# Optimization experiments

Hardware: AMD Instinct MI355X
Metric: run time of the kernel (lower is better)

## Reference

```python
import jax, jax.numpy as jnp
import numpy as np

NUM_HEADS = 32
MAX_BIAS_LENGTH = 1024
ROPE_BASE = 10000.0


def _rope_cos_sin(seq_len, head_dim, dtype):
    half = head_dim // 2
    inv_freq = 1.0 / (ROPE_BASE ** (jnp.arange(0, half, dtype=jnp.float32) / half))
    t = jnp.arange(seq_len, dtype=jnp.float32)
    freqs = jnp.outer(t, inv_freq)  # [S, half]
    return jnp.cos(freqs).astype(dtype), jnp.sin(freqs).astype(dtype)


def _apply_rope(x, cos, sin):
    # x: [B, S, H, D]; non-interleaved (GPT-NeoX / flash-attn style) rotary
    half = x.shape[-1] // 2
    x1, x2 = x[..., :half], x[..., half:]
    c = cos[None, :, None, :]
    s = sin[None, :, None, :]
    return jnp.concatenate([x1 * c - x2 * s, x1 * s + x2 * c], axis=-1)


def setup_inputs() -> dict:
    key = jax.random.key(0)
    ks = jax.random.split(key, 7)
    B, S, Dm = 2, 2048, 2048
    std = 1.0 / np.sqrt(Dm)
    return {
        "hidden_states": jax.random.normal(ks[0], (B, S, Dm), jnp.float32),
        "Wq": jax.random.normal(ks[1], (Dm, Dm), jnp.float32) * std,
        "Wk": jax.random.normal(ks[2], (Dm, Dm), jnp.float32) * std,
        "Wv": jax.random.normal(ks[3], (Dm, Dm), jnp.float32) * std,
        "Wo": jax.random.normal(ks[4], (Dm, Dm), jnp.float32) * std,
        "learnable_bias": jax.random.normal(ks[5], (NUM_HEADS, MAX_BIAS_LENGTH), jnp.float32) * 0.001,
        "softmax_offset": jnp.zeros((NUM_HEADS,), jnp.float32),
    }


def reference(hidden_states, Wq, Wk, Wv, Wo, learnable_bias, softmax_offset):
    B, S, Dm = hidden_states.shape
    H = NUM_HEADS
    D = Dm // H
    scale = D ** -0.5

    # projections (nn.Linear: x @ W.T)
    q = (hidden_states @ Wq.T).reshape(B, S, H, D)
    k = (hidden_states @ Wk.T).reshape(B, S, H, D)
    v = (hidden_states @ Wv.T).reshape(B, S, H, D)

    cos, sin = _rope_cos_sin(S, D, q.dtype)
    q = _apply_rope(q, cos, sin)
    k = _apply_rope(k, cos, sin)

    q = q.transpose(0, 2, 1, 3)  # [B, H, S, D]
    k = k.transpose(0, 2, 1, 3)
    v = v.transpose(0, 2, 1, 3)

    scores = jnp.einsum("bhid,bhjd->bhij", q, k) * scale  # [B, H, S, S]

    # per-diagonal learnable bias: diag = i - j in [0, MAX_BIAS_LENGTH)
    i = jnp.arange(S)[:, None]
    j = jnp.arange(S)[None, :]
    diag = i - j  # [S, S]
    causal = diag >= 0
    in_band = causal & (diag < MAX_BIAS_LENGTH)
    bias = jnp.where(in_band, learnable_bias[:, jnp.clip(diag, 0, MAX_BIAS_LENGTH - 1)], 0.0)  # [H, S, S]
    scores = scores + bias[None]
    scores = jnp.where(causal[None, None], scores, -jnp.inf)

    # softmax with learnable per-head offset (attention-sink logit)
    off = softmax_offset[None, :, None]  # [1, H, 1]
    m = jnp.maximum(jnp.max(scores, axis=-1), off)  # [B, H, S]
    p = jnp.exp(scores - m[..., None])
    denom = jnp.sum(p, axis=-1) + jnp.exp(off - m)  # [B, H, S]
    out = jnp.einsum("bhij,bhjd->bhid", p, v) / denom[..., None]

    out = out.transpose(0, 2, 1, 3).reshape(B, S, Dm)
    return out @ Wo.T
```

## Files before the change

### kernel.cpp

```cpp
#include <hip/hip_runtime.h>
#include <hip/hip_bf16.h>
#include <stdint.h>

typedef __bf16 bf16x8 __attribute__((ext_vector_type(8)));
typedef float f32x4 __attribute__((ext_vector_type(4)));
typedef unsigned short u16;
typedef u16 u16x4 __attribute__((ext_vector_type(4)));

#define S_LEN 2048
#define DMODEL 2048
#define NHEADS 32
#define BATCH 2
#define MROWS (BATCH * S_LEN)
#define BIAS_LEN 1024
#define LOG2E 1.44269504088896f

__device__ __forceinline__ u16 b16(float f) {
  union { __bf16 h; u16 u; } cv; cv.h = (__bf16)f; return cv.u;
}

__device__ __forceinline__ void gload16(const void* g, void* l) {
  __builtin_amdgcn_global_load_lds(
      (const __attribute__((address_space(1))) uint32_t*)g,
      (__attribute__((address_space(3))) uint32_t*)l, 16, 0, 0);
}

__global__ __launch_bounds__(256)
void prep_all(const float* __restrict__ hs,
              const float* __restrict__ w0, const float* __restrict__ w1,
              const float* __restrict__ w2, const float* __restrict__ w3,
              const float* __restrict__ bias,
              u16* __restrict__ hs_b, u16* __restrict__ w_b,
              float* __restrict__ ct, float* __restrict__ st,
              u16* __restrict__ b16t)
{
  const int blk = blockIdx.x;
  if (blk < 8192) {
    int i = (blk * 256 + threadIdx.x) * 4;
    float4 v = *(const float4*)(hs + i);
    u16x4 o = { b16(v.x), b16(v.y), b16(v.z), b16(v.w) };
    *(u16x4*)(hs_b + i) = o;
  } else if (blk < 24576) {
    int r = blk - 8192;
    int which = r >> 12;
    const float* src = (which == 0) ? w0 : (which == 1) ? w1
                     : (which == 2) ? w2 : w3;
    int i = ((r & 4095) * 256 + threadIdx.x) * 4;
    float4 v = *(const float4*)(src + i);
    u16x4 o = { b16(v.x), b16(v.y), b16(v.z), b16(v.w) };
    *(u16x4*)(w_b + (size_t)which * DMODEL * DMODEL + i) = o;
  } else if (blk < 24832) {
    int idx = (blk - 24576) * 256 + threadIdx.x;
    int s = idx >> 5, d = idx & 31;
    float inv = exp2f((float)d * (-13.287712379549449f / 32.0f));
    float a = (float)s * inv;
    ct[idx] = cosf(a);
    st[idx] = sinf(a);
  } else {
    int i = (blk - 24832) * 256 + threadIdx.x;
    b16t[i] = b16(bias[i] * LOG2E);
  }
}

#define GEMM_MAIN_LOOP(Aptr, Bptr)                                            \
  f32x4 acc[4][4] = {};                                                       \
  const u16* aS[4]; const u16* bS[4];                                         \
  _Pragma("unroll")                                                           \
  for (int it = 0; it < 4; ++it) {                                            \
    int u = it * 256 + tid;                                                   \
    int row = u >> 3;                                                         \
    int ch  = (u & 7) ^ (row & 7);                                            \
    aS[it] = (Aptr) + (size_t)(tm + row) * DMODEL + ch * 8;                   \
    bS[it] = (Bptr) + (size_t)(tn + row) * DMODEL + ch * 8;                   \
  }                                                                           \
  for (int k0 = 0; k0 < DMODEL; k0 += 64) {                                   \
    __syncthreads();                                                          \
    _Pragma("unroll")                                                         \
    for (int it = 0; it < 4; ++it) {                                          \
      int u = it * 256 + tid;                                                 \
      gload16(aS[it] + k0, (char*)sA + u * 16);                               \
      gload16(bS[it] + k0, (char*)sB + u * 16);                               \
    }                                                                         \
    __syncthreads();                                                          \
    _Pragma("unroll")                                                         \
    for (int kk = 0; kk < 2; ++kk) {                                          \
      bf16x8 af[4], bq[4];                                                    \
      _Pragma("unroll")                                                       \
      for (int mi = 0; mi < 4; ++mi) {                                        \
        int row = wm * 64 + mi * 16 + lc;                                     \
        int ch  = (kk * 4 + lr) ^ (row & 7);                                  \
        af[mi] = *(const bf16x8*)((const char*)sA + row * 128 + ch * 16);     \
      }                                                                       \
      _Pragma("unroll")                                                       \
      for (int ni = 0; ni < 4; ++ni) {                                        \
        int row = wn * 64 + ni * 16 + lc;                                     \
        int ch  = (kk * 4 + lr) ^ (row & 7);                                  \
        bq[ni] = *(const bf16x8*)((const char*)sB + row * 128 + ch * 16);     \
      }                                                                       \
      _Pragma("unroll")                                                       \
      for (int mi = 0; mi < 4; ++mi)                                          \
        _Pragma("unroll")                                                     \
        for (int ni = 0; ni < 4; ++ni)                                        \
          acc[mi][ni] = __builtin_amdgcn_mfma_f32_16x16x32_bf16(              \
              af[mi], bq[ni], acc[mi][ni], 0, 0, 0);                          \
    }                                                                         \
  }

__global__ __launch_bounds__(256)
void gemm_qkv(const u16* __restrict__ A, const u16* __restrict__ W,
              u16* __restrict__ qf, u16* __restrict__ kf, u16* __restrict__ vt,
              const float* __restrict__ ctab, const float* __restrict__ stab)
{
  __shared__ u16 sA[128 * 64];
  __shared__ u16 sB[128 * 64];
  const int tid  = threadIdx.x;
  const int lane = tid & 63;
  const int wid  = tid >> 6;
  const int wm   = wid >> 1, wn = wid & 1;
  const int lc   = lane & 15, lr = lane >> 4;
  const int L = blockIdx.x;
  const int r = L >> 3;
  const int x = (L & 7) * 6 + (r % 6);
  const int y = r / 6;
  const int which = x >> 4;
  const int tn = (x & 15) * 128;
  const int tm = y * 128;
  const u16* Bm = W + (size_t)which * DMODEL * DMODEL;

  GEMM_MAIN_LOOP(A, Bm)

  if (which == 2) {
    u16* C = vt;
#pragma unroll
    for (int mi = 0; mi < 4; ++mi)
#pragma unroll
      for (int ni = 0; ni < 4; ++ni) {
        int col = tn + wn * 64 + ni * 16 + lc;
        int hh = col >> 6, d = col & 63;
        int m0 = tm + wm * 64 + mi * 16 + lr * 4;
        int bb = m0 >> 11, s = m0 & 2047;
        u16x4 v = { b16(acc[mi][ni][0]), b16(acc[mi][ni][1]),
                    b16(acc[mi][ni][2]), b16(acc[mi][ni][3]) };
        *(u16x4*)(C + (((size_t)bb * NHEADS + hh) * 64 + d) * S_LEN + s) = v;
      }
  } else {
    u16* C = (which == 0) ? qf : kf;
    const float scl = (which == 0) ? 0.125f * LOG2E : 1.0f;
#pragma unroll
    for (int mi = 0; mi < 4; ++mi)
#pragma unroll
      for (int ni = 0; ni < 2; ++ni)
#pragma unroll
        for (int j = 0; j < 4; ++j) {
          int col = tn + wn * 64 + ni * 16 + lc;
          int hh = col >> 6, dl = col & 63;
          int rr2 = tm + wm * 64 + mi * 16 + lr * 4 + j;
          int bb = rr2 >> 11, s = rr2 & 2047;
          float x1 = acc[mi][ni][j], x2 = acc[mi][ni + 2][j];
          float cv = ctab[s * 32 + dl], sv = stab[s * 32 + dl];
          float o1 = (x1 * cv - x2 * sv) * scl;
          float o2 = (x1 * sv + x2 * cv) * scl;
          size_t base = (((size_t)bb * NHEADS + hh) * S_LEN + s) * 64 + dl;
          C[base]      = b16(o1);
          C[base + 32] = b16(o2);
        }
  }
}

__global__ __launch_bounds__(256)
void gemm_out(const u16* __restrict__ A, const u16* __restrict__ Bm,
              float* __restrict__ C)
{
  __shared__ u16 sA[128 * 64];
  __shared__ u16 sB[128 * 64];
  const int tid  = threadIdx.x;
  const int lane = tid & 63;
  const int wid  = tid >> 6;
  const int wm   = wid >> 1, wn = wid & 1;
  const int lc   = lane & 15, lr = lane >> 4;
  const int L = blockIdx.x;
  const int r = L >> 3;
  const int x = (L & 7) * 2 + (r & 1);
  const int y = r >> 1;
  const int tn = x * 128;
  const int tm = y * 128;

  GEMM_MAIN_LOOP(A, Bm)

#pragma unroll
  for (int mi = 0; mi < 4; ++mi)
#pragma unroll
    for (int ni = 0; ni < 4; ++ni)
#pragma unroll
      for (int j = 0; j < 4; ++j) {
        int rr2 = tm + wm * 64 + mi * 16 + lr * 4 + j;
        int c = tn + wn * 64 + ni * 16 + lc;
        C[(size_t)rr2 * DMODEL + c] = acc[mi][ni][j];
      }
}

__global__ __launch_bounds__(512, 6)
void attn_kernel(const u16* __restrict__ Q, const u16* __restrict__ K,
                 const u16* __restrict__ V, const u16* __restrict__ bias16,
                 const float* __restrict__ offg, u16* __restrict__ O)
{
  __shared__ __align__(16) u16 sK[2][64 * 64];
  __shared__ __align__(16) u16 sV[2][64 * 64];
  __shared__ __align__(16) u16 sP[8][16 * 72];
  __shared__ __align__(8)  u16 sBiasT[1152];

  const int tid = threadIdx.x, lane = tid & 63, wid = tid >> 6;
  const int lc = lane & 15, lr = lane >> 4;
  const int L  = blockIdx.x;
  const int p  = 15 - (L >> 6);
  const int bh = L & 63;
  const int h  = bh & 31;
  const int b  = bh >> 5;
  const int qw = p * 128 + wid * 16;
  const int nt = 2 * p + 2;

  for (int i = tid; i < 1152; i += 512) {
    int dd = i - 64;
    sBiasT[i] = (dd >= 0 && dd < BIAS_LEN) ? bias16[h * BIAS_LEN + dd] : (u16)0;
  }
  const float off = offg[h] * LOG2E;

  const u16* qp = Q + ((size_t)bh * S_LEN + qw + lc) * 64;
  bf16x8 aq0 = *(const bf16x8*)(qp + lr * 8);
  bf16x8 aq1 = *(const bf16x8*)(qp + 32 + lr * 8);

  const int srow = tid >> 3;
  const int sch  = (tid & 7) ^ (srow & 7);
  const u16* kSrc = K + ((size_t)bh * S_LEN + srow) * 64 + sch * 8;
  const u16* vSrc = V + ((size_t)bh * 64 + srow) * S_LEN + sch * 8;

  int offK[4][2], offV[2][4];
#pragma unroll
  for (int f = 0; f < 4; ++f) {
    int row = f * 16 + lc;
    offK[f][0] = row * 128 + ((lr) ^ (row & 7)) * 16;
    offK[f][1] = row * 128 + ((4 + lr) ^ (row & 7)) * 16;
  }
#pragma unroll
  for (int kk = 0; kk < 2; ++kk)
#pragma unroll
    for (int f2 = 0; f2 < 4; ++f2) {
      int drow = f2 * 16 + lc;
      offV[kk][f2] = drow * 128 + ((kk * 4 + lr) ^ (drow & 7)) * 16;
    }

  float lsum = 0.0f;
  f32x4 o[4] = {};

  gload16(kSrc, (char*)sK[0] + tid * 16);
  gload16(vSrc, (char*)sV[0] + tid * 16);
  __syncthreads();

  for (int t = 0; t < nt; ++t) {
    const int cur = t & 1;
    if (t + 1 < nt) {
      gload16(kSrc + (size_t)(t + 1) * 4096, (char*)sK[cur ^ 1] + tid * 16);
      gload16(vSrc + (t + 1) * 64,           (char*)sV[cur ^ 1] + tid * 16);
    }

    const int dqt = qw - t * 64;
    if (dqt >= 0) {
      const int db = dqt + lc;
      const bool inband = (dqt < 1088);
      f32x4 sc[4];
      __builtin_amdgcn_s_setprio(1);
#pragma unroll
      for (int f = 0; f < 4; ++f) {
        f32x4 z;
        if (inband) {
          const int ib = db + 64 - lr * 4 - f * 16;
#pragma unroll
          for (int j = 0; j < 4; ++j)
            z[j] = __uint_as_float((uint32_t)sBiasT[ib - j] << 16);
        } else {
          z[0] = z[1] = z[2] = z[3] = 0.0f;
        }
        bf16x8 k0 = *(const bf16x8*)((const char*)sK[cur] + offK[f][0]);
        bf16x8 k1 = *(const bf16x8*)((const char*)sK[cur] + offK[f][1]);
        z     = __builtin_amdgcn_mfma_f32_16x16x32_bf16(k0, aq0, z, 0, 0, 0);
        sc[f] = __builtin_amdgcn_mfma_f32_16x16x32_bf16(k1, aq1, z, 0, 0, 0);
      }
      __builtin_amdgcn_s_setprio(0);

      float pvv[4][4];
      if (dqt < 64) {
#pragma unroll
        for (int f = 0; f < 4; ++f)
#pragma unroll
          for (int j = 0; j < 4; ++j) {
            int dd = db - (f * 16 + lr * 4 + j);
            pvv[f][j] = (dd >= 0) ? sc[f][j] : -1e30f;
          }
      } else {
#pragma unroll
        for (int f = 0; f < 4; ++f)
#pragma unroll
          for (int j = 0; j < 4; ++j) pvv[f][j] = sc[f][j];
      }
#pragma unroll
      for (int f = 0; f < 4; ++f)
#pragma unroll
        for (int j = 0; j < 4; ++j) {
          float pe = exp2f(pvv[f][j]);
          pvv[f][j] = pe;
          lsum += pe;
        }

      u16* myP = sP[wid];
#pragma unroll
      for (int f = 0; f < 4; ++f) {
        u16x4 w = { b16(pvv[f][0]), b16(pvv[f][1]), b16(pvv[f][2]), b16(pvv[f][3]) };
        *(u16x4*)(myP + lc * 72 + f * 16 + lr * 4) = w;
      }
      asm volatile("s_waitcnt lgkmcnt(0)" ::: "memory");
      __builtin_amdgcn_sched_barrier(0);
      bf16x8 ap0 = *(const bf16x8*)(myP + lc * 72 + lr * 8);
      bf16x8 ap1 = *(const bf16x8*)(myP + lc * 72 + 32 + lr * 8);
      __builtin_amdgcn_s_setprio(1);
#pragma unroll
      for (int f2 = 0; f2 < 4; ++f2) {
        bf16x8 bv = *(const bf16x8*)((const char*)sV[cur] + offV[0][f2]);
        o[f2] = __builtin_amdgcn_mfma_f32_16x16x32_bf16(ap0, bv, o[f2], 0, 0, 0);
      }
#pragma unroll
      for (int f2 = 0; f2 < 4; ++f2) {
        bf16x8 bv = *(const bf16x8*)((const char*)sV[cur] + offV[1][f2]);
        o[f2] = __builtin_amdgcn_mfma_f32_16x16x32_bf16(ap1, bv, o[f2], 0, 0, 0);
      }
      __builtin_amdgcn_s_setprio(0);
    }
    __syncthreads();
  }

  lsum += __shfl_xor(lsum, 16, 64);
  lsum += __shfl_xor(lsum, 32, 64);
  lsum += exp2f(off);
  float ls[4];
#pragma unroll
  for (int j = 0; j < 4; ++j) ls[j] = 1.0f / __shfl(lsum, lr * 4 + j, 64);
#pragma unroll
  for (int f2 = 0; f2 < 4; ++f2)
#pragma unroll
    for (int j = 0; j < 4; ++j) {
      int i = qw + lr * 4 + j;
      int d = f2 * 16 + lc;
      size_t addr = (((size_t)(b * S_LEN + i)) * NHEADS + h) * 64 + d;
      O[addr] = b16(o[f2][j] * ls[j]);
    }
}

extern "C" void kernel_launch(void* const* d_in, const int* in_sizes, int n_in,
                              void* d_out, int out_size, void* d_ws, size_t ws_size,
                              hipStream_t stream)
{
  const float* hs   = (const float*)d_in[0];
  const float* Wq   = (const float*)d_in[1];
  const float* Wk   = (const float*)d_in[2];
  const float* Wv   = (const float*)d_in[3];
  const float* Wo   = (const float*)d_in[4];
  const float* bias = (const float*)d_in[5];
  const float* off  = (const float*)d_in[6];

  char* p = (char*)d_ws;
  u16* hs_b = (u16*)p; p += (size_t)MROWS * DMODEL * 2;
  u16* wq_b = (u16*)p; p += (size_t)DMODEL * DMODEL * 2;
  u16* wk_b = (u16*)p; p += (size_t)DMODEL * DMODEL * 2;
  u16* wv_b = (u16*)p; p += (size_t)DMODEL * DMODEL * 2;
  u16* wo_b = (u16*)p; p += (size_t)DMODEL * DMODEL * 2;
  u16* qf   = (u16*)p; p += (size_t)MROWS * DMODEL * 2;
  u16* kf   = (u16*)p; p += (size_t)MROWS * DMODEL * 2;
  u16* vt   = (u16*)p; p += (size_t)MROWS * DMODEL * 2;
  u16* att  = (u16*)p; p += (size_t)MROWS * DMODEL * 2;
  float* ct = (float*)p; p += (size_t)S_LEN * 32 * 4;
  float* st = (float*)p; p += (size_t)S_LEN * 32 * 4;
  u16* b16t = (u16*)p; p += (size_t)NHEADS * BIAS_LEN * 2;
  (void)ws_size; (void)in_sizes; (void)n_in; (void)out_size;
  (void)wk_b; (void)wv_b;

  prep_all<<<dim3(24960), 256, 0, stream>>>(hs, Wq, Wk, Wv, Wo, bias,
                                            hs_b, wq_b, ct, st, b16t);
  gemm_qkv<<<dim3(1536), 256, 0, stream>>>(hs_b, wq_b, qf, kf, vt, ct, st);
  attn_kernel<<<dim3(16 * 64), 512, 0, stream>>>(qf, kf, vt, b16t, off, att);
  gemm_out<<<dim3(512), 256, 0, stream>>>(att, wo_b, (float*)d_out);
}
```

Measured before the change: 274.3 us.

## Process two 128-row query groups per attention block to reuse K/V tiles

Each attention block now handles 256 query rows, split into two interleaved 128-row groups, so every wave computes two 16-row query tiles. Each K/V tile loaded into shared memory is reused by both groups, and the V fragments are read once and fed to both PV MFMAs. This halves the block count and cuts K/V global-to-LDS traffic per query. In exchange it raises register pressure (occupancy hint lowered from 6 to 4) and doubles the P scratch space. A scheduling remap pairs long and short causal rows.

```diff
diff --git a/kernel.cpp b/kernel.cpp
--- a/kernel.cpp
+++ b/kernel.cpp
@@ -199,25 +199,26 @@
       }
 }
 
-__global__ __launch_bounds__(512, 6)
+__global__ __launch_bounds__(512, 4)
 void attn_kernel(const u16* __restrict__ Q, const u16* __restrict__ K,
                  const u16* __restrict__ V, const u16* __restrict__ bias16,
                  const float* __restrict__ offg, u16* __restrict__ O)
 {
   __shared__ __align__(16) u16 sK[2][64 * 64];
   __shared__ __align__(16) u16 sV[2][64 * 64];
-  __shared__ __align__(16) u16 sP[8][16 * 72];
+  __shared__ __align__(16) u16 sP[16][16 * 72];
   __shared__ __align__(8)  u16 sBiasT[1152];
 
   const int tid = threadIdx.x, lane = tid & 63, wid = tid >> 6;
   const int lc = lane & 15, lr = lane >> 4;
   const int L  = blockIdx.x;
-  const int p  = 15 - (L >> 6);
+  const int sidx = L >> 6;
+  const int p  = (sidx < 4) ? 7 - sidx : sidx - 4;
   const int bh = L & 63;
   const int h  = bh & 31;
   const int b  = bh >> 5;
-  const int qw = p * 128 + wid * 16;
-  const int nt = 2 * p + 2;
+  const int qw0 = p * 256 + wid * 16;
+  const int nt = 4 * p + 4;
 
   for (int i = tid; i < 1152; i += 512) {
     int dd = i - 64;
@@ -225,9 +226,11 @@
   }
   const float off = offg[h] * LOG2E;
 
-  const u16* qp = Q + ((size_t)bh * S_LEN + qw + lc) * 64;
-  bf16x8 aq0 = *(const bf16x8*)(qp + lr * 8);
-  bf16x8 aq1 = *(const bf16x8*)(qp + 32 + lr * 8);
+  const u16* qp0 = Q + ((size_t)bh * S_LEN + qw0 + lc) * 64;
+  bf16x8 aq00 = *(const bf16x8*)(qp0 + lr * 8);
+  bf16x8 aq01 = *(const bf16x8*)(qp0 + 32 + lr * 8);
+  bf16x8 aq10 = *(const bf16x8*)(qp0 + 128 * 64 + lr * 8);
+  bf16x8 aq11 = *(const bf16x8*)(qp0 + 128 * 64 + 32 + lr * 8);
 
   const int srow = tid >> 3;
   const int sch  = (tid & 7) ^ (srow & 7);
@@ -249,12 +252,66 @@
       offV[kk][f2] = drow * 128 + ((kk * 4 + lr) ^ (drow & 7)) * 16;
     }
 
-  float lsum = 0.0f;
-  f32x4 o[4] = {};
+  float lsum0 = 0.0f, lsum1 = 0.0f;
+  f32x4 o0[4] = {}, o1[4] = {};
 
   gload16(kSrc, (char*)sK[0] + tid * 16);
   gload16(vSrc, (char*)sV[0] + tid * 16);
   __syncthreads();
+
+  auto do_group = [&](int dqt, const bf16x8& q0, const bf16x8& q1,
+                      u16* myP, float& lsum, const u16* sKc) {
+    const int db = dqt + lc;
+    const bool inband = (dqt < 1088);
+    f32x4 sc[4];
+    __builtin_amdgcn_s_setprio(1);
+#pragma unroll
+    for (int f = 0; f < 4; ++f) {
+      f32x4 z;
+      if (inband) {
+        const int ib = db + 64 - lr * 4 - f * 16;
+#pragma unroll
+        for (int j = 0; j < 4; ++j)
+          z[j] = __uint_as_float((uint32_t)sBiasT[ib - j] << 16);
+      } else {
+        z[0] = z[1] = z[2] = z[3] = 0.0f;
+      }
+      bf16x8 k0 = *(const bf16x8*)((const char*)sKc + offK[f][0]);
+      bf16x8 k1 = *(const bf16x8*)((const char*)sKc + offK[f][1]);
+      z     = __builtin_amdgcn_mfma_f32_16x16x32_bf16(k0, q0, z, 0, 0, 0);
+      sc[f] = __builtin_amdgcn_mfma_f32_16x16x32_bf16(k1, q1, z, 0, 0, 0);
+    }
+    __builtin_amdgcn_s_setprio(0);
+
+    float pvv[4][4];
+    if (dqt < 64) {
+#pragma unroll
+      for (int f = 0; f < 4; ++f)
+#pragma unroll
+        for (int j = 0; j < 4; ++j) {
+          int dd = db - (f * 16 + lr * 4 + j);
+          pvv[f][j] = (dd >= 0) ? sc[f][j] : -1e30f;
+        }
+    } else {
+#pragma unroll
+      for (int f = 0; f < 4; ++f)
+#pragma unroll
+        for (int j = 0; j < 4; ++j) pvv[f][j] = sc[f][j];
+    }
+#pragma unroll
+    for (int f = 0; f < 4; ++f)
+#pragma unroll
+      for (int j = 0; j < 4; ++j) {
+        float pe = exp2f(pvv[f][j]);
+        pvv[f][j] = pe;
+        lsum += pe;
+      }
+#pragma unroll
+    for (int f = 0; f < 4; ++f) {
+      u16x4 w = { b16(pvv[f][0]), b16(pvv[f][1]), b16(pvv[f][2]), b16(pvv[f][3]) };
+      *(u16x4*)(myP + lc * 72 + f * 16 + lr * 4) = w;
+    }
+  };
 
   for (int t = 0; t < nt; ++t) {
     const int cur = t & 1;
@@ -263,94 +320,63 @@
       gload16(vSrc + (t + 1) * 64,           (char*)sV[cur ^ 1] + tid * 16);
     }
 
-    const int dqt = qw - t * 64;
-    if (dqt >= 0) {
-      const int db = dqt + lc;
-      const bool inband = (dqt < 1088);
-      f32x4 sc[4];
+    const int dqt0 = qw0 - t * 64;
+    const int dqt1 = dqt0 + 128;
+    const bool a0 = (dqt0 >= 0), a1 = (dqt1 >= 0);
+
+    if (a1) do_group(dqt1, aq10, aq11, sP[wid * 2 + 1], lsum1, sK[cur]);
+    if (a0) do_group(dqt0, aq00, aq01, sP[wid * 2 + 0], lsum0, sK[cur]);
+
+    if (a1) {
+      asm volatile("s_waitcnt lgkmcnt(0)" ::: "memory");
+      __builtin_amdgcn_sched_barrier(0);
+      u16* P0 = sP[wid * 2 + 0];
+      u16* P1 = sP[wid * 2 + 1];
       __builtin_amdgcn_s_setprio(1);
 #pragma unroll
-      for (int f = 0; f < 4; ++f) {
-        f32x4 z;
-        if (inband) {
-          const int ib = db + 64 - lr * 4 - f * 16;
-#pragma unroll
-          for (int j = 0; j < 4; ++j)
-            z[j] = __uint_as_float((uint32_t)sBiasT[ib - j] << 16);
-        } else {
-          z[0] = z[1] = z[2] = z[3] = 0.0f;
+      for (int kk = 0; kk < 2; ++kk) {
+        bf16x8 bv[4];
+#pragma unroll
+        for (int f2 = 0; f2 < 4; ++f2)
+          bv[f2] = *(const bf16x8*)((const char*)sV[cur] + offV[kk][f2]);
+        bf16x8 ap1 = *(const bf16x8*)(P1 + lc * 72 + kk * 32 + lr * 8);
+#pragma unroll
+        for (int f2 = 0; f2 < 4; ++f2)
+          o1[f2] = __builtin_amdgcn_mfma_f32_16x16x32_bf16(ap1, bv[f2], o1[f2], 0, 0, 0);
+        if (a0) {
+          bf16x8 ap0 = *(const bf16x8*)(P0 + lc * 72 + kk * 32 + lr * 8);
+#pragma unroll
+          for (int f2 = 0; f2 < 4; ++f2)
+            o0[f2] = __builtin_amdgcn_mfma_f32_16x16x32_bf16(ap0, bv[f2], o0[f2], 0, 0, 0);
         }
-        bf16x8 k0 = *(const bf16x8*)((const char*)sK[cur] + offK[f][0]);
-        bf16x8 k1 = *(const bf16x8*)((const char*)sK[cur] + offK[f][1]);
-        z     = __builtin_amdgcn_mfma_f32_16x16x32_bf16(k0, aq0, z, 0, 0, 0);
-        sc[f] = __builtin_amdgcn_mfma_f32_16x16x32_bf16(k1, aq1, z, 0, 0, 0);
       }
       __builtin_amdgcn_s_setprio(0);
-
-      float pvv[4][4];
-      if (dqt < 64) {
-#pragma unroll
-        for (int f = 0; f < 4; ++f)
-#pragma unroll
-          for (int j = 0; j < 4; ++j) {
-            int dd = db - (f * 16 + lr * 4 + j);
-            pvv[f][j] = (dd >= 0) ? sc[f][j] : -1e30f;
-          }
-      } else {
-#pragma unroll
-        for (int f = 0; f < 4; ++f)
-#pragma unroll
-          for (int j = 0; j < 4; ++j) pvv[f][j] = sc[f][j];
-      }
-#pragma unroll
-      for (int f = 0; f < 4; ++f)
-#pragma unroll
-        for (int j = 0; j < 4; ++j) {
-          float pe = exp2f(pvv[f][j]);
-          pvv[f][j] = pe;
-          lsum += pe;
-        }
-
-      u16* myP = sP[wid];
-#pragma unroll
-      for (int f = 0; f < 4; ++f) {
-        u16x4 w = { b16(pvv[f][0]), b16(pvv[f][1]), b16(pvv[f][2]), b16(pvv[f][3]) };
-        *(u16x4*)(myP + lc * 72 + f * 16 + lr * 4) = w;
-      }
-      asm volatile("s_waitcnt lgkmcnt(0)" ::: "memory");
-      __builtin_amdgcn_sched_barrier(0);
-      bf16x8 ap0 = *(const bf16x8*)(myP + lc * 72 + lr * 8);
-      bf16x8 ap1 = *(const bf16x8*)(myP + lc * 72 + 32 + lr * 8);
-      __builtin_amdgcn_s_setprio(1);
-#pragma unroll
-      for (int f2 = 0; f2 < 4; ++f2) {
-        bf16x8 bv = *(const bf16x8*)((const char*)sV[cur] + offV[0][f2]);
-        o[f2] = __builtin_amdgcn_mfma_f32_16x16x32_bf16(ap0, bv, o[f2], 0, 0, 0);
-      }
-#pragma unroll
-      for (int f2 = 0; f2 < 4; ++f2) {
-        bf16x8 bv = *(const bf16x8*)((const char*)sV[cur] + offV[1][f2]);
-        o[f2] = __builtin_amdgcn_mfma_f32_16x16x32_bf16(ap1, bv, o[f2], 0, 0, 0);
-      }
-      __builtin_amdgcn_s_setprio(0);
     }
     __syncthreads();
   }
 
-  lsum += __shfl_xor(lsum, 16, 64);
-  lsum += __shfl_xor(lsum, 32, 64);
-  lsum += exp2f(off);
-  float ls[4];
-#pragma unroll
-  for (int j = 0; j < 4; ++j) ls[j] = 1.0f / __shfl(lsum, lr * 4 + j, 64);
+  lsum0 += __shfl_xor(lsum0, 16, 64);
+  lsum0 += __shfl_xor(lsum0, 32, 64);
+  lsum0 += exp2f(off);
+  lsum1 += __shfl_xor(lsum1, 16, 64);
+  lsum1 += __shfl_xor(lsum1, 32, 64);
+  lsum1 += exp2f(off);
+  float ls0[4], ls1[4];
+#pragma unroll
+  for (int j = 0; j < 4; ++j) {
+    ls0[j] = 1.0f / __shfl(lsum0, lr * 4 + j, 64);
+    ls1[j] = 1.0f / __shfl(lsum1, lr * 4 + j, 64);
+  }
 #pragma unroll
   for (int f2 = 0; f2 < 4; ++f2)
 #pragma unroll
     for (int j = 0; j < 4; ++j) {
-      int i = qw + lr * 4 + j;
+      int i0 = qw0 + lr * 4 + j;
       int d = f2 * 16 + lc;
-      size_t addr = (((size_t)(b * S_LEN + i)) * NHEADS + h) * 64 + d;
-      O[addr] = b16(o[f2][j] * ls[j]);
+      size_t a0d = (((size_t)(b * S_LEN + i0)) * NHEADS + h) * 64 + d;
+      O[a0d] = b16(o0[f2][j] * ls0[j]);
+      size_t a1d = (((size_t)(b * S_LEN + i0 + 128)) * NHEADS + h) * 64 + d;
+      O[a1d] = b16(o1[f2][j] * ls1[j]);
     }
 }
 
@@ -385,6 +411,6 @@
   prep_all<<<dim3(24960), 256, 0, stream>>>(hs, Wq, Wk, Wv, Wo, bias,
                                             hs_b, wq_b, ct, st, b16t);
   gemm_qkv<<<dim3(1536), 256, 0, stream>>>(hs_b, wq_b, qf, kf, vt, ct, st);
-  attn_kernel<<<dim3(16 * 64), 512, 0, stream>>>(qf, kf, vt, b16t, off, att);
+  attn_kernel<<<dim3(512), 512, 0, stream>>>(qf, kf, vt, b16t, off, att);
   gemm_out<<<dim3(512), 256, 0, stream>>>(att, wo_b, (float*)d_out);
 }
```

Result: no change. 276.3 us (+0.7%).

## Split QKV GEMM into 256x256 double-buffered Q/K kernel and separate V GEMM

Applied to the files above, without the earlier changes.

Replaces the single fused QKV projection kernel with a new Q/K GEMM that uses 256x256 tiles, 512 threads, a double-buffered LDS pipeline with explicit vmcnt/lgkmcnt waits, barriers and MFMA priority boosting. V is moved to its own 128x128 GEMM kernel. The aim is more data reuse per tile and better overlap of global loads with MFMA work. The cost is an extra kernel launch, large LDS use that limits occupancy, and only 256 blocks for the Q/K part, which may leave CUs underused.

```diff
diff --git a/kernel.cpp b/kernel.cpp
--- a/kernel.cpp
+++ b/kernel.cpp
@@ -60,6 +60,121 @@
     int i = (blk - 24832) * 256 + threadIdx.x;
     b16t[i] = b16(bias[i] * LOG2E);
   }
+}
+
+#define NT 32
+
+#define STG_A(buf, h, t) { \
+    gload16(aS0 + (size_t)(h) * 128 * DMODEL + (t) * 64, (char*)sA[buf][h] + tid * 16); \
+    gload16(aS0 + (size_t)((h) * 128 + 64) * DMODEL + (t) * 64, (char*)sA[buf][h] + (512 + tid) * 16); }
+#define STG_B(buf, h, t) { \
+    gload16(bS0 + (size_t)(h) * 128 * DMODEL + (t) * 64, (char*)sB[buf][h] + tid * 16); \
+    gload16(bS0 + (size_t)((h) * 128 + 64) * DMODEL + (t) * 64, (char*)sB[buf][h] + (512 + tid) * 16); }
+#define LOAD_B(b, kk) { _Pragma("unroll") \
+    for (int ni = 0; ni < 4; ++ni) \
+      bq[ni] = *(const bf16x8*)((const char*)sB[b][wn >> 1] + offB[ni][kk]); }
+#define LOAD_A(b, q, kk) { _Pragma("unroll") \
+    for (int mi = 0; mi < 4; ++mi) \
+      af[mi] = *(const bf16x8*)((const char*)sA[b][wm] + offA[q][mi][kk]); }
+#define MFMA16(q) { __builtin_amdgcn_s_setprio(1); \
+    _Pragma("unroll") for (int mi = 0; mi < 4; ++mi) \
+      _Pragma("unroll") for (int ni = 0; ni < 4; ++ni) \
+        acc[(q) * 4 + mi][ni] = __builtin_amdgcn_mfma_f32_16x16x32_bf16( \
+            af[mi], bq[ni], acc[(q) * 4 + mi][ni], 0, 0, 0); \
+    __builtin_amdgcn_s_setprio(0); }
+#define LGKM { asm volatile("s_waitcnt lgkmcnt(0)" ::: "memory"); \
+               __builtin_amdgcn_sched_barrier(0); }
+#define BARR { __builtin_amdgcn_s_barrier(); __builtin_amdgcn_sched_barrier(0); }
+#define VM2 { asm volatile("s_waitcnt vmcnt(2)" ::: "memory"); \
+              __builtin_amdgcn_sched_barrier(0); }
+#define VM0 { asm volatile("s_waitcnt vmcnt(0)" ::: "memory"); \
+              __builtin_amdgcn_sched_barrier(0); }
+
+__global__ __launch_bounds__(512, 2)
+void gemm_qk8(const u16* __restrict__ A, const u16* __restrict__ W,
+              u16* __restrict__ qf, u16* __restrict__ kf,
+              const float* __restrict__ ctab, const float* __restrict__ stab)
+{
+  __shared__ u16 sA[2][2][128 * 64];
+  __shared__ u16 sB[2][2][128 * 64];
+  const int tid = threadIdx.x, lane = tid & 63, wid = tid >> 6;
+  const int wm = wid >> 2, wn = wid & 3;
+  const int lc = lane & 15, lr = lane >> 4;
+  const int L = blockIdx.x;
+  const int which = L >> 7;
+  const int rr = L & 127;
+  const int tmi = rr >> 3, tni = rr & 7;
+  const size_t tm = (size_t)tmi * 256, tn = (size_t)tni * 256;
+  const u16* Bm = W + (size_t)which * DMODEL * DMODEL;
+
+  const int r0 = tid >> 3, c0 = (tid & 7) ^ (r0 & 7);
+  const u16* aS0 = A  + (tm + r0) * DMODEL + c0 * 8;
+  const u16* bS0 = Bm + (tn + r0) * DMODEL + c0 * 8;
+
+  int offA[2][4][2], offB[4][2];
+#pragma unroll
+  for (int q = 0; q < 2; ++q)
+#pragma unroll
+    for (int mi = 0; mi < 4; ++mi) {
+      int row = q * 64 + mi * 16 + lc;
+#pragma unroll
+      for (int kk = 0; kk < 2; ++kk)
+        offA[q][mi][kk] = row * 128 + ((kk * 4 + lr) ^ (row & 7)) * 16;
+    }
+#pragma unroll
+  for (int ni = 0; ni < 4; ++ni) {
+    int row = (wn & 1) * 64 + ni * 16 + lc;
+#pragma unroll
+    for (int kk = 0; kk < 2; ++kk)
+      offB[ni][kk] = row * 128 + ((kk * 4 + lr) ^ (row & 7)) * 16;
+  }
+
+  f32x4 acc[8][4] = {};
+  bf16x8 af[4], bq[4];
+
+  STG_B(0, 0, 0); STG_B(0, 1, 0); STG_A(0, 0, 0); STG_A(0, 1, 0); STG_B(1, 0, 1);
+  VM2; BARR;
+
+  for (int i = 0; i < NT / 2; ++i) {
+    const int t1 = 2 * i + 1, t2 = 2 * i + 2, t3 = 2 * i + 3;
+    LOAD_B(0, 0); LOAD_A(0, 0, 0); STG_B(1, 1, t1); LGKM; MFMA16(0);
+    LOAD_A(0, 1, 0); STG_A(1, 0, t1); LGKM; MFMA16(1);
+    LOAD_B(0, 1); LOAD_A(0, 0, 1); STG_A(1, 1, t1); LGKM; MFMA16(0);
+    BARR;
+    LOAD_A(0, 1, 1); if (t2 < NT) STG_B(0, 0, t2); LGKM; MFMA16(1);
+    if (t2 < NT) { VM2; } else { VM0; }
+    BARR;
+    LOAD_B(1, 0); LOAD_A(1, 0, 0); if (t2 < NT) STG_B(0, 1, t2); LGKM; MFMA16(0);
+    LOAD_A(1, 1, 0); if (t2 < NT) STG_A(0, 0, t2); LGKM; MFMA16(1);
+    LOAD_B(1, 1); LOAD_A(1, 0, 1); if (t2 < NT) STG_A(0, 1, t2); LGKM; MFMA16(0);
+    BARR;
+    LOAD_A(1, 1, 1); if (t3 < NT) STG_B(1, 0, t3); LGKM; MFMA16(1);
+    if (t3 < NT) { VM2; } else { VM0; }
+    BARR;
+  }
+
+  u16* C = (which == 0) ? qf : kf;
+  const float scl = (which == 0) ? 0.125f * LOG2E : 1.0f;
+#pragma unroll
+  for (int q = 0; q < 2; ++q)
+#pragma unroll
+    for (int mi = 0; mi < 4; ++mi)
+#pragma unroll
+      for (int ni = 0; ni < 2; ++ni)
+#pragma unroll
+        for (int j = 0; j < 4; ++j) {
+          int col = (int)tn + wn * 64 + ni * 16 + lc;
+          int hh = col >> 6, dl = col & 63;
+          int r = (int)tm + wm * 128 + q * 64 + mi * 16 + lr * 4 + j;
+          int bb = r >> 11, s = r & 2047;
+          float x1 = acc[q * 4 + mi][ni][j], x2 = acc[q * 4 + mi][ni + 2][j];
+          float cv = ctab[s * 32 + dl], sv = stab[s * 32 + dl];
+          float o1 = (x1 * cv - x2 * sv) * scl;
+          float o2 = (x1 * sv + x2 * cv) * scl;
+          size_t base = (((size_t)bb * NHEADS + hh) * S_LEN + s) * 64 + dl;
+          C[base]      = b16(o1);
+          C[base + 32] = b16(o2);
+        }
 }
 
 #define GEMM_MAIN_LOOP(Aptr, Bptr)                                            \
@@ -107,9 +222,8 @@
   }
 
 __global__ __launch_bounds__(256)
-void gemm_qkv(const u16* __restrict__ A, const u16* __restrict__ W,
-              u16* __restrict__ qf, u16* __restrict__ kf, u16* __restrict__ vt,
-              const float* __restrict__ ctab, const float* __restrict__ stab)
+void gemm_v(const u16* __restrict__ A, const u16* __restrict__ Bm,
+            u16* __restrict__ vt)
 {
   __shared__ u16 sA[128 * 64];
   __shared__ u16 sB[128 * 64];
@@ -120,51 +234,25 @@
   const int lc   = lane & 15, lr = lane >> 4;
   const int L = blockIdx.x;
   const int r = L >> 3;
-  const int x = (L & 7) * 6 + (r % 6);
-  const int y = r / 6;
-  const int which = x >> 4;
-  const int tn = (x & 15) * 128;
+  const int x = (L & 7) * 2 + (r & 1);
+  const int y = r >> 1;
+  const int tn = x * 128;
   const int tm = y * 128;
-  const u16* Bm = W + (size_t)which * DMODEL * DMODEL;
 
   GEMM_MAIN_LOOP(A, Bm)
 
-  if (which == 2) {
-    u16* C = vt;
-#pragma unroll
-    for (int mi = 0; mi < 4; ++mi)
-#pragma unroll
-      for (int ni = 0; ni < 4; ++ni) {
-        int col = tn + wn * 64 + ni * 16 + lc;
-        int hh = col >> 6, d = col & 63;
-        int m0 = tm + wm * 64 + mi * 16 + lr * 4;
-        int bb = m0 >> 11, s = m0 & 2047;
-        u16x4 v = { b16(acc[mi][ni][0]), b16(acc[mi][ni][1]),
-                    b16(acc[mi][ni][2]), b16(acc[mi][ni][3]) };
-        *(u16x4*)(C + (((size_t)bb * NHEADS + hh) * 64 + d) * S_LEN + s) = v;
-      }
-  } else {
-    u16* C = (which == 0) ? qf : kf;
-    const float scl = (which == 0) ? 0.125f * LOG2E : 1.0f;
-#pragma unroll
-    for (int mi = 0; mi < 4; ++mi)
-#pragma unroll
-      for (int ni = 0; ni < 2; ++ni)
-#pragma unroll
-        for (int j = 0; j < 4; ++j) {
-          int col = tn + wn * 64 + ni * 16 + lc;
-          int hh = col >> 6, dl = col & 63;
-          int rr2 = tm + wm * 64 + mi * 16 + lr * 4 + j;
-          int bb = rr2 >> 11, s = rr2 & 2047;
-          float x1 = acc[mi][ni][j], x2 = acc[mi][ni + 2][j];
-          float cv = ctab[s * 32 + dl], sv = stab[s * 32 + dl];
-          float o1 = (x1 * cv - x2 * sv) * scl;
-          float o2 = (x1 * sv + x2 * cv) * scl;
-          size_t base = (((size_t)bb * NHEADS + hh) * S_LEN + s) * 64 + dl;
-          C[base]      = b16(o1);
-          C[base + 32] = b16(o2);
-        }
-  }
+#pragma unroll
+  for (int mi = 0; mi < 4; ++mi)
+#pragma unroll
+    for (int ni = 0; ni < 4; ++ni) {
+      int col = tn + wn * 64 + ni * 16 + lc;
+      int hh = col >> 6, d = col & 63;
+      int m0 = tm + wm * 64 + mi * 16 + lr * 4;
+      int bb = m0 >> 11, s = m0 & 2047;
+      u16x4 v = { b16(acc[mi][ni][0]), b16(acc[mi][ni][1]),
+                  b16(acc[mi][ni][2]), b16(acc[mi][ni][3]) };
+      *(u16x4*)(vt + (((size_t)bb * NHEADS + hh) * 64 + d) * S_LEN + s) = v;
+    }
 }
 
 __global__ __launch_bounds__(256)
@@ -380,11 +468,12 @@
   float* st = (float*)p; p += (size_t)S_LEN * 32 * 4;
   u16* b16t = (u16*)p; p += (size_t)NHEADS * BIAS_LEN * 2;
   (void)ws_size; (void)in_sizes; (void)n_in; (void)out_size;
-  (void)wk_b; (void)wv_b;
+  (void)wk_b;
 
   prep_all<<<dim3(24960), 256, 0, stream>>>(hs, Wq, Wk, Wv, Wo, bias,
                                             hs_b, wq_b, ct, st, b16t);
-  gemm_qkv<<<dim3(1536), 256, 0, stream>>>(hs_b, wq_b, qf, kf, vt, ct, st);
+  gemm_qk8<<<dim3(256), 512, 0, stream>>>(hs_b, wq_b, qf, kf, ct, st);
+  gemm_v<<<dim3(512), 256, 0, stream>>>(hs_b, wv_b, vt);
   attn_kernel<<<dim3(16 * 64), 512, 0, stream>>>(qf, kf, vt, b16t, off, att);
   gemm_out<<<dim3(512), 256, 0, stream>>>(att, wo_b, (float*)d_out);
 }
```

Result: no change. 269.0 us (-1.9%).
